# Performance work log

Hardware: AMD Instinct MI355X
Metric: run time of the kernel (lower is better)

## Reference

```python
import jax, jax.numpy as jnp
import numpy as np

B, T, E, H, V = 64, 64, 512, 512, 32000

def setup_inputs() -> dict:
    key = jax.random.key(0)
    ks = jax.random.split(key, 12)
    s_e = 1.0 / np.sqrt(E)
    s_h = 1.0 / np.sqrt(H)
    embed_table = jax.random.normal(ks[0], (V, E), jnp.float32) * 0.02
    embed_table = embed_table.at[0].set(0.0)  # padding_idx=0
    return {
        "enc_feats": jax.random.normal(ks[1], (B, E), jnp.float32),
        "captions": jax.random.randint(ks[2], (B, T), 1, V),
        "embed_table": embed_table,
        "W_ih": jax.random.normal(ks[3], (4 * H, E), jnp.float32) * s_e,
        "W_hh": jax.random.normal(ks[4], (4 * H, H), jnp.float32) * s_h,
        "b_ih": jax.random.normal(ks[5], (4 * H,), jnp.float32) * s_h,
        "b_hh": jax.random.normal(ks[6], (4 * H,), jnp.float32) * s_h,
        "Wh": jax.random.normal(ks[7], (H, E), jnp.float32) * s_e,
        "bh": jnp.zeros((H,), jnp.float32),
        "Wc": jax.random.normal(ks[8], (H, E), jnp.float32) * s_e,
        "bc": jnp.zeros((H,), jnp.float32),
        "Wout": jax.random.normal(ks[9], (V, H), jnp.float32) * s_h,
        "bout": jnp.zeros((V,), jnp.float32),
    }


def reference(enc_feats, captions, embed_table, W_ih, W_hh, b_ih, b_hh, Wh, bh, Wc, bc, Wout, bout):
    # Teacher-forced decode (forward_train, eval mode -> dropout is identity).
    inputs = captions[:, :-1]                       # [B, T-1]
    emb = embed_table[inputs]                       # [B, T-1, E]
    # Precompute input contribution to gates for all timesteps.
    xp = jnp.einsum("bte,ge->btg", emb, W_ih) + b_ih  # [B, T-1, 4H]
    xp = jnp.transpose(xp, (1, 0, 2))                 # [T-1, B, 4H]
    h0 = jnp.tanh(enc_feats @ Wh.T + bh)              # [B, H]
    c0 = jnp.tanh(enc_feats @ Wc.T + bc)              # [B, H]

    def step(carry, x_t):
        h, c = carry
        gates = x_t + h @ W_hh.T + b_hh               # [B, 4H]
        i, f, g, o = jnp.split(gates, 4, axis=-1)     # PyTorch gate order i,f,g,o
        i = jax.nn.sigmoid(i)
        f = jax.nn.sigmoid(f)
        g = jnp.tanh(g)
        o = jax.nn.sigmoid(o)
        c = f * c + i * g
        h = o * jnp.tanh(c)
        return (h, c), h

    _, hs = jax.lax.scan(step, (h0, c0), xp)          # hs: [T-1, B, H]
    logits = jnp.einsum("tbh,vh->btv", hs, Wout) + bout  # [B, T-1, V]
    return logits
```

## Files before the change

kernel.cpp:

```cpp
#include <hip/hip_runtime.h>
#include <hip/hip_bf16.h>
#include <stdint.h>
#include <math.h>

typedef __attribute__((ext_vector_type(4))) float f32x4;
typedef __attribute__((ext_vector_type(8))) short short8;

#define NB 64
#define NT 63
#define NE 512
#define NH 512
#define NV 32000
#define NG 2048
#define GQ 4
#define GS 16

__device__ __forceinline__ float sigm(float x) { return 1.f / (1.f + expf(-x)); }
__device__ __forceinline__ unsigned short f2b(float f) {
  union { float f; uint32_t u; } x; x.f = f;
  uint32_t r = x.u + 0x7FFF + ((x.u >> 16) & 1);
  return (unsigned short)(r >> 16);
}
__device__ __forceinline__ float b2f(unsigned short s) {
  union { uint32_t u; float f; } x; x.u = ((uint32_t)s) << 16; return x.f;
}
__device__ __forceinline__ f32x4 mfma16(short8 a, short8 b, f32x4 c) {
  return __builtin_amdgcn_mfma_f32_16x16x32_bf16(a, b, c, 0, 0, 0);
}

__global__ __launch_bounds__(256) void k_prep(
    const float* __restrict__ Wout, unsigned short* __restrict__ wb,
    unsigned short* __restrict__ hsb) {
  const int n4 = NV * NH / 4;
  for (int i = blockIdx.x * 256 + threadIdx.x; i < n4; i += gridDim.x * 256) {
    f32x4 v = *(const f32x4*)(Wout + (size_t)i * 4);
    unsigned short o[4];
#pragma unroll
    for (int u = 0; u < 4; ++u) o[u] = f2b(v[u]);
    *(uint64_t*)(wb + (size_t)i * 4) = *(const uint64_t*)o;
  }
  for (int i = blockIdx.x * 256 + threadIdx.x; i < 64 * NH; i += gridDim.x * 256)
    hsb[(size_t)(NT * NB) * NH + i] = 0;
}

__global__ __launch_bounds__(256) void k_prep2(
    const float* __restrict__ Whh, unsigned short* __restrict__ wp) {
  const int n4 = NG * NH / 4;
  for (int i4 = blockIdx.x * 256 + threadIdx.x; i4 < n4; i4 += gridDim.x * 256) {
    int r = i4 >> 7;
    int k4 = (i4 & 127) * 4;
    int np = 4 * (r & 511) + (r >> 9);
    f32x4 v = *(const f32x4*)(Whh + (size_t)r * NH + k4);
    unsigned short o[4];
#pragma unroll
    for (int u = 0; u < 4; ++u) o[u] = f2b(v[u]);
    *(uint64_t*)(wp + (size_t)np * NH + k4) = *(const uint64_t*)o;
  }
}

__global__ __launch_bounds__(256) void k_init(
    const float* __restrict__ enc, const float* __restrict__ Wh, const float* __restrict__ bh,
    const float* __restrict__ Wc, const float* __restrict__ bc,
    float* __restrict__ c0f, unsigned short* __restrict__ hAhi, unsigned short* __restrict__ hAlo) {
  int b = blockIdx.x;
  __shared__ float se[NE];
  for (int e = threadIdx.x; e < NE; e += 256) se[e] = enc[b * NE + e];
  __syncthreads();
  for (int j = threadIdx.x; j < NH; j += 256) {
    float dh = 0.f, dc = 0.f;
    const float* wh = Wh + (size_t)j * NE;
    const float* wc = Wc + (size_t)j * NE;
    for (int e = 0; e < NE; e += 4) {
      f32x4 vh = *(const f32x4*)(wh + e);
      f32x4 vc = *(const f32x4*)(wc + e);
#pragma unroll
      for (int u = 0; u < 4; ++u) {
        float x = se[e + u];
        dh += x * vh[u];
        dc += x * vc[u];
      }
    }
    float h = tanhf(dh + bh[j]);
    unsigned short hi = f2b(h);
    hAhi[b * NH + j] = hi;
    hAlo[b * NH + j] = f2b(h - b2f(hi));
    c0f[b * NH + j] = tanhf(dc + bc[j]);
  }
}

__global__ __launch_bounds__(256) void k_xp(
    const int* __restrict__ cap, const float* __restrict__ emb,
    const float* __restrict__ Wih, const float* __restrict__ bih, const float* __restrict__ bhh,
    float* __restrict__ xp) {
  int t = blockIdx.x;
  int g0 = blockIdx.y * 64;
  int b = threadIdx.x & 63;
  int gg = threadIdx.x >> 6;
  __shared__ float wl[64 * 32];

  int tok = cap[b * 64 + t];
  const float* er = emb + (size_t)tok * NE;

  float acc[16];
#pragma unroll
  for (int i = 0; i < 16; ++i) acc[i] = 0.f;

  for (int k0 = 0; k0 < NE; k0 += 32) {
    __syncthreads();
#pragma unroll
    for (int i = 0; i < 2; ++i) {
      int s = threadIdx.x + 256 * i;
      int gr = s >> 3, c4 = s & 7;
      *(f32x4*)(wl + gr * 32 + c4 * 4) =
          *(const f32x4*)(Wih + (size_t)(g0 + gr) * NE + k0 + c4 * 4);
    }
    __syncthreads();
    f32x4 e4[8];
#pragma unroll
    for (int u = 0; u < 8; ++u) e4[u] = *(const f32x4*)(er + k0 + u * 4);
#pragma unroll
    for (int k4 = 0; k4 < 8; ++k4) {
#pragma unroll
      for (int i = 0; i < 16; ++i) {
        f32x4 w = *(const f32x4*)(wl + (gg * 16 + i) * 32 + k4 * 4);
#pragma unroll
        for (int u = 0; u < 4; ++u) acc[i] += e4[k4][u] * w[u];
      }
    }
  }
  size_t rb = ((size_t)(t * NB) + b) * NG;
#pragma unroll
  for (int i = 0; i < 16; ++i) {
    int g = g0 + gg * 16 + i;
    int np = 4 * (g & 511) + (g >> 9);
    xp[rb + np] = acc[i] + bih[g] + bhh[g];
  }
}

__global__ __launch_bounds__(512, 1) void k_steps_p(
    const float* __restrict__ xp, const unsigned short* __restrict__ wp,
    unsigned short* __restrict__ hAhi, unsigned short* __restrict__ hAlo,
    unsigned short* __restrict__ hBhi, unsigned short* __restrict__ hBlo,
    const float* __restrict__ c0f, unsigned short* __restrict__ hsb,
    int* __restrict__ syncc) {
  int tid = threadIdx.x;
  int lane = tid & 63;
  int w = tid >> 6;
  int l15 = lane & 15;
  int kq = lane >> 4;
  int q = blockIdx.x >> 4;
  int s = blockIdx.x & 15;
  int m0 = q * 16;
  int ju = tid & 31;
  int mu = tid >> 5;
  int J = s * 32 + ju;

  __shared__ unsigned short hh[16 * 512];
  __shared__ unsigned short hl[16 * 512];
  __shared__ float gb[128][17];

  float creg = c0f[(size_t)(m0 + mu) * NH + J];
  int* cnt = syncc + q * 32;
  const unsigned short* wpw = wp + ((size_t)s * 128 + w * 16 + l15) * 512;

  for (int t = 0; t < NT; ++t) {
    const unsigned short* rhi = (t & 1) ? hBhi : hAhi;
    const unsigned short* rlo = (t & 1) ? hBlo : hAlo;
    unsigned short* whi2 = (t & 1) ? hAhi : hBhi;
    unsigned short* wlo2 = (t & 1) ? hAlo : hBlo;

    f32x4 x4 = *(const f32x4*)(xp + ((size_t)t * NB + m0 + mu) * NG + 4 * J);

#pragma unroll
    for (int rdd = 0; rdd < 2; ++rdd) {
      int idx = tid + rdd * 512;
      int m = idx >> 6;
      int ke = (idx & 63) * 8;
      int d = m * 512 + (ke ^ (8 * (m & 7)));
      *(short8*)(hh + d) = *(const short8*)(rhi + (size_t)(m0 + m) * 512 + ke);
      *(short8*)(hl + d) = *(const short8*)(rlo + (size_t)(m0 + m) * 512 + ke);
    }
    __syncthreads();

    f32x4 acc = (f32x4){0.f, 0.f, 0.f, 0.f};
    for (int ks = 0; ks < 16; ++ks) {
      int k = ks * 32 + kq * 8;
      short8 bf = *(const short8*)(wpw + k);
      int aoff = l15 * 512 + (k ^ (8 * (l15 & 7)));
      acc = mfma16(*(const short8*)(hh + aoff), bf, acc);
      acc = mfma16(*(const short8*)(hl + aoff), bf, acc);
    }

#pragma unroll
    for (int r = 0; r < 4; ++r)
      gb[w * 16 + l15][kq * 4 + r] = acc[r];
    __syncthreads();

    float g0 = gb[4 * ju + 0][mu];
    float g1 = gb[4 * ju + 1][mu];
    float g2 = gb[4 * ju + 2][mu];
    float g3 = gb[4 * ju + 3][mu];
    float gi = g0 + x4[0];
    float gf = g1 + x4[1];
    float gG = g2 + x4[2];
    float go = g3 + x4[3];
    float cn = sigm(gf) * creg + sigm(gi) * tanhf(gG);
    creg = cn;
    float h = sigm(go) * tanhf(cn);
    unsigned short hi = f2b(h);
    size_t hoff = (size_t)(m0 + mu) * NH + J;
    whi2[hoff] = hi;
    wlo2[hoff] = f2b(h - b2f(hi));
    hsb[(size_t)t * NB * NH + hoff] = hi;

    if (t < NT - 1) {
      __syncthreads();
      if (tid == 0) {
        __threadfence();
        __hip_atomic_fetch_add(cnt, 1, __ATOMIC_RELEASE, __HIP_MEMORY_SCOPE_AGENT);
        while (__hip_atomic_load(cnt, __ATOMIC_ACQUIRE, __HIP_MEMORY_SCOPE_AGENT)
               < GS * (t + 1)) {}
        __threadfence();
      }
      __syncthreads();
    }
  }
}

__global__ __launch_bounds__(256) void k_logits_m(
    const unsigned short* __restrict__ hsb, const unsigned short* __restrict__ wb,
    const float* __restrict__ bout, float* __restrict__ out) {
  __shared__ unsigned short As[128 * 64];
  __shared__ unsigned short Bs[128 * 64];
  __shared__ float cst[4][16][68];
  int m0 = blockIdx.x * 128;
  int n0 = blockIdx.y * 128;
  int tid = threadIdx.x;
  int lane = tid & 63;
  int l15 = lane & 15;
  int kl = (lane >> 4) * 8;
  int w = tid >> 6;
  int wr = w >> 1, wc = w & 1;

  f32x4 acc[4][4];
#pragma unroll
  for (int i = 0; i < 4; ++i)
#pragma unroll
    for (int j = 0; j < 4; ++j) acc[i][j] = (f32x4){0.f, 0.f, 0.f, 0.f};

  for (int k0 = 0; k0 < NH; k0 += 64) {
    short8 ta[4], tb[4];
#pragma unroll
    for (int cc = 0; cc < 4; ++cc) {
      int idx = cc * 2048 + tid * 8;
      int row = idx >> 6;
      int ke = idx & 63;
      ta[cc] = *(const short8*)(hsb + (size_t)(m0 + row) * NH + k0 + ke);
      tb[cc] = *(const short8*)(wb + (size_t)(n0 + row) * NH + k0 + ke);
    }
    __syncthreads();
#pragma unroll
    for (int cc = 0; cc < 4; ++cc) {
      int idx = cc * 2048 + tid * 8;
      int row = idx >> 6;
      int ke = (idx & 63) ^ ((row & 7) << 3);
      *(short8*)(As + row * 64 + ke) = ta[cc];
      *(short8*)(Bs + row * 64 + ke) = tb[cc];
    }
    __syncthreads();
#pragma unroll
    for (int kk = 0; kk < 64; kk += 32) {
      short8 a[4], b[4];
#pragma unroll
      for (int mi = 0; mi < 4; ++mi) {
        int row = wr * 64 + mi * 16 + l15;
        a[mi] = *(const short8*)(As + row * 64 + ((kk + kl) ^ ((row & 7) << 3)));
      }
#pragma unroll
      for (int ni = 0; ni < 4; ++ni) {
        int row = wc * 64 + ni * 16 + l15;
        b[ni] = *(const short8*)(Bs + row * 64 + ((kk + kl) ^ ((row & 7) << 3)));
      }
#pragma unroll
      for (int mi = 0; mi < 4; ++mi)
#pragma unroll
        for (int ni = 0; ni < 4; ++ni)
          acc[mi][ni] = mfma16(a[mi], b[ni], acc[mi][ni]);
    }
  }

  f32x4 bo4 = *(const f32x4*)(bout + n0 + wc * 64 + l15 * 4);
#pragma unroll
  for (int mi = 0; mi < 4; ++mi) {
    __syncthreads();
#pragma unroll
    for (int ni = 0; ni < 4; ++ni)
#pragma unroll
      for (int r = 0; r < 4; ++r)
        cst[w][(lane >> 4) * 4 + r][ni * 16 + l15] = acc[mi][ni][r];
    __syncthreads();
#pragma unroll
    for (int p = 0; p < 4; ++p) {
      int row16 = p * 4 + (lane >> 4);
      int m = m0 + wr * 64 + mi * 16 + row16;
      f32x4 v = *(const f32x4*)&cst[w][row16][l15 * 4];
#pragma unroll
      for (int u = 0; u < 4; ++u) v[u] += bo4[u];
      if (m < NT * NB) {
        int t = m >> 6, b = m & 63;
        *(f32x4*)(out + (size_t)b * (NT * NV) + (size_t)t * NV + n0 + wc * 64 + l15 * 4) = v;
      }
    }
  }
}

extern "C" void kernel_launch(void* const* d_in, const int* in_sizes, int n_in,
                              void* d_out, int out_size, void* d_ws, size_t ws_size,
                              hipStream_t stream) {
  const float* enc  = (const float*)d_in[0];
  const int*   cap  = (const int*)d_in[1];
  const float* emb  = (const float*)d_in[2];
  const float* Wih  = (const float*)d_in[3];
  const float* Whh  = (const float*)d_in[4];
  const float* bih  = (const float*)d_in[5];
  const float* bhh  = (const float*)d_in[6];
  const float* Wh   = (const float*)d_in[7];
  const float* bh   = (const float*)d_in[8];
  const float* Wc   = (const float*)d_in[9];
  const float* bc   = (const float*)d_in[10];
  const float* Wout = (const float*)d_in[11];
  const float* bout = (const float*)d_in[12];
  float* out = (float*)d_out;

  char* ws = (char*)d_ws;
  constexpr size_t HA_HI = 0;
  constexpr size_t HA_LO = HA_HI + 65536;
  constexpr size_t HB_HI = HA_LO + 65536;
  constexpr size_t HB_LO = HB_HI + 65536;
  constexpr size_t HSB_OFF = HB_LO + 65536;
  constexpr size_t WB_OFF  = HSB_OFF + (size_t)4096 * NH * 2;
  constexpr size_t WP_OFF  = WB_OFF + (size_t)NV * NH * 2;
  constexpr size_t XP_OFF  = WP_OFF + (size_t)NG * NH * 2;
  unsigned short* hAhi = (unsigned short*)(ws + HA_HI);
  unsigned short* hAlo = (unsigned short*)(ws + HA_LO);
  unsigned short* hBhi = (unsigned short*)(ws + HB_HI);
  unsigned short* hBlo = (unsigned short*)(ws + HB_LO);
  float* c0f = (float*)(ws + HB_HI);
  unsigned short* hsb = (unsigned short*)(ws + HSB_OFF);
  unsigned short* wb  = (unsigned short*)(ws + WB_OFF);
  unsigned short* wp  = (unsigned short*)(ws + WP_OFF);
  float* xp = (float*)(ws + XP_OFF);
  int* syncc = (int*)(ws + HSB_OFF + (size_t)(NT * NB) * NH * 2);

  k_prep<<<1024, 256, 0, stream>>>(Wout, wb, hsb);
  k_prep2<<<256, 256, 0, stream>>>(Whh, wp);
  k_init<<<NB, 256, 0, stream>>>(enc, Wh, bh, Wc, bc, c0f, hAhi, hAlo);

  dim3 g2(NT, NG / 64);
  k_xp<<<g2, 256, 0, stream>>>(cap, emb, Wih, bih, bhh, xp);

  k_steps_p<<<GQ * GS, 512, 0, stream>>>(xp, wp, hAhi, hAlo, hBhi, hBlo, c0f, hsb, syncc);

  dim3 g4(32, NV / 128);
  k_logits_m<<<g4, 256, 0, stream>>>(hsb, wb, bout, out);
}
```

Measured before the change: 1.129 ms.

## Keep recurrent weights in registers, read h directly, remap logits block order

The recurrent step kernel now loads its W_hh fragment into registers once, before the time loop, instead of re-reading it from global memory every step. The h hi/lo operands are read straight from global memory rather than staged through swizzled LDS, which removes one __syncthreads per step. The gate exchange buffer is transposed so each thread reads its four gates as a single vector load. Separately, the logits GEMM remaps block IDs with a swizzle that groups blocks sharing an n-tile across XCDs to improve L2 reuse; this uses more registers in the step kernel and trades LDS reads for uncoalesced-ish global reads.

```diff
diff --git a/kernel.cpp b/kernel.cpp
--- a/kernel.cpp
+++ b/kernel.cpp
@@ -155,13 +155,19 @@
   int mu = tid >> 5;
   int J = s * 32 + ju;
 
-  __shared__ unsigned short hh[16 * 512];
-  __shared__ unsigned short hl[16 * 512];
-  __shared__ float gb[128][17];
+  __shared__ float gbf[16 * 132];
 
   float creg = c0f[(size_t)(m0 + mu) * NH + J];
   int* cnt = syncc + q * 32;
-  const unsigned short* wpw = wp + ((size_t)s * 128 + w * 16 + l15) * 512;
+
+  short8 bfr[16];
+  {
+    const unsigned short* wpw = wp + ((size_t)s * 128 + w * 16 + l15) * 512;
+#pragma unroll
+    for (int ks = 0; ks < 16; ++ks)
+      bfr[ks] = *(const short8*)(wpw + ks * 32 + kq * 8);
+  }
+  const size_t arow = (size_t)(m0 + l15) * 512 + kq * 8;
 
   for (int t = 0; t < NT; ++t) {
     const unsigned short* rhi = (t & 1) ? hBhi : hAhi;
@@ -171,39 +177,25 @@
 
     f32x4 x4 = *(const f32x4*)(xp + ((size_t)t * NB + m0 + mu) * NG + 4 * J);
 
-#pragma unroll
-    for (int rdd = 0; rdd < 2; ++rdd) {
-      int idx = tid + rdd * 512;
-      int m = idx >> 6;
-      int ke = (idx & 63) * 8;
-      int d = m * 512 + (ke ^ (8 * (m & 7)));
-      *(short8*)(hh + d) = *(const short8*)(rhi + (size_t)(m0 + m) * 512 + ke);
-      *(short8*)(hl + d) = *(const short8*)(rlo + (size_t)(m0 + m) * 512 + ke);
-    }
-    __syncthreads();
-
     f32x4 acc = (f32x4){0.f, 0.f, 0.f, 0.f};
+#pragma unroll
     for (int ks = 0; ks < 16; ++ks) {
-      int k = ks * 32 + kq * 8;
-      short8 bf = *(const short8*)(wpw + k);
-      int aoff = l15 * 512 + (k ^ (8 * (l15 & 7)));
-      acc = mfma16(*(const short8*)(hh + aoff), bf, acc);
-      acc = mfma16(*(const short8*)(hl + aoff), bf, acc);
+      short8 ahi = *(const short8*)(rhi + arow + ks * 32);
+      short8 alo = *(const short8*)(rlo + arow + ks * 32);
+      acc = mfma16(ahi, bfr[ks], acc);
+      acc = mfma16(alo, bfr[ks], acc);
     }
 
 #pragma unroll
     for (int r = 0; r < 4; ++r)
-      gb[w * 16 + l15][kq * 4 + r] = acc[r];
-    __syncthreads();
-
-    float g0 = gb[4 * ju + 0][mu];
-    float g1 = gb[4 * ju + 1][mu];
-    float g2 = gb[4 * ju + 2][mu];
-    float g3 = gb[4 * ju + 3][mu];
-    float gi = g0 + x4[0];
-    float gf = g1 + x4[1];
-    float gG = g2 + x4[2];
-    float go = g3 + x4[3];
+      gbf[(kq * 4 + r) * 132 + w * 16 + l15] = acc[r];
+    __syncthreads();
+
+    f32x4 g4 = *(const f32x4*)(gbf + mu * 132 + 4 * ju);
+    float gi = g4[0] + x4[0];
+    float gf = g4[1] + x4[1];
+    float gG = g4[2] + x4[2];
+    float go = g4[3] + x4[3];
     float cn = sigm(gf) * creg + sigm(gi) * tanhf(gG);
     creg = cn;
     float h = sigm(go) * tanhf(cn);
@@ -233,8 +225,10 @@
   __shared__ unsigned short As[128 * 64];
   __shared__ unsigned short Bs[128 * 64];
   __shared__ float cst[4][16][68];
-  int m0 = blockIdx.x * 128;
-  int n0 = blockIdx.y * 128;
+  int bid = blockIdx.x + 32 * blockIdx.y;
+  int swz = (bid & 7) * 1000 + (bid >> 3);
+  int m0 = (swz & 31) * 128;
+  int n0 = (swz >> 5) * 128;
   int tid = threadIdx.x;
   int lane = tid & 63;
   int l15 = lane & 15;
```

After: 1.435 ms. 27.1% more time.
